# Kernel optimization log

Hardware: AMD Instinct MI355X
Metric: run time of the kernel (lower is better)

## Reference

```python
import jax, jax.numpy as jnp
import numpy as np

N = 100000      # nodes
E = 1600000     # edges
D_IN = 128
D_H = 128
D_OUT = 32
NUM_LAYERS = 3


def setup_inputs() -> dict:
    key = jax.random.key(0)
    ks = jax.random.split(key, 12)
    x = jax.random.normal(ks[0], (N, D_IN), dtype=jnp.float32)
    edge_index = jax.random.randint(ks[1], (2, E), 0, N, dtype=jnp.int64)
    def lin(k, fan_in, fan_out):
        bound = 1.0 / np.sqrt(fan_in)
        kw, kb = jax.random.split(k)
        W = jax.random.uniform(kw, (fan_in, fan_out), jnp.float32, -bound, bound)
        b = jax.random.uniform(kb, (fan_out,), jnp.float32, -bound, bound)
        return W, b
    W0, b0 = lin(ks[2], D_IN, D_H)
    W1, b1 = lin(ks[3], D_H, D_H)
    W2, b2 = lin(ks[4], D_H, D_H)
    Wfc, bfc = lin(ks[5], D_H, D_OUT)
    return {"x": x, "edge_index": edge_index, "W0": W0, "b0": b0,
            "W1": W1, "b1": b1, "W2": W2, "b2": b2, "Wfc": Wfc, "bfc": bfc}


def reference(x, edge_index, W0, b0, W1, b1, W2, b2, Wfc, bfc):
    n = x.shape[0]
    # add self-loops once (PyG GCNConv default add_self_loops=True)
    loop = jnp.arange(n, dtype=edge_index.dtype)
    src = jnp.concatenate([edge_index[0], loop])  # [E+N]
    dst = jnp.concatenate([edge_index[1], loop])
    # symmetric degree normalization: deg computed over destination (col)
    deg = jax.ops.segment_sum(jnp.ones_like(dst, dtype=x.dtype), dst, num_segments=n)
    dis = jnp.where(deg > 0, jax.lax.rsqrt(deg), 0.0)  # deg^{-1/2}, inf->0
    norm = (dis[src] * dis[dst])[:, None]              # [E+N, 1]

    def gcn_conv(h, W, b):
        h = h @ W                                       # [N, d_out]
        agg = jax.ops.segment_sum(h[src] * norm, dst, num_segments=n)
        return agg + b                                  # bias after aggregation

    h = x
    for (W, b) in ((W0, b0), (W1, b1), (W2, b2)):
        h = jax.nn.relu(gcn_conv(h, W, b))              # dropout p=0 -> identity
    pooled = jnp.mean(h, axis=0)                        # [D_H]
    return pooled @ Wfc + bfc                           # [D_OUT]
```

## Files before the change

### kernel.cpp

```cpp
#include <hip/hip_runtime.h>
#include <hip/hip_bf16.h>
#include <cstdint>


typedef unsigned short u16;
typedef unsigned int u32;
typedef unsigned char u8;
typedef __attribute__((ext_vector_type(8))) short short8v;
typedef __attribute__((ext_vector_type(4))) float f32x4;
typedef __attribute__((ext_vector_type(2))) float f32x2;

#define NBMAX 256
#define BKSH  9
#define SCH   2048
#define CAP   12288

__device__ inline u16 f2bf(float f) {
  u32 u = __float_as_uint(f);
  u += 0x7fff + ((u >> 16) & 1);
  return (u16)(u >> 16);
}
__device__ inline float bflo(u32 u) { return __uint_as_float(u << 16); }
__device__ inline float bfhi(u32 u) { return __uint_as_float(u & 0xffff0000u); }

__global__ void k_init(const int* __restrict__ ei, int* __restrict__ mode,
                       int* __restrict__ bucketCur, float* __restrict__ pooled,
                       int e, int nb) {
  if (blockIdx.x == 0) {
    __shared__ int any;
    if (threadIdx.x == 0) any = 0;
    __syncthreads();
    int lim = min(e, 2048);
    int local = 0;
    for (int i = threadIdx.x; i < lim; i += blockDim.x)
      local |= (ei[2 * i + 1] != 0);
    if (local) atomicOr(&any, 1);
    __syncthreads();
    if (threadIdx.x == 0) mode[0] = (any == 0) ? 1 : 0;
  } else {
    int i = threadIdx.x;
    if (i < nb) bucketCur[i] = 0;
    if (i < 128) pooled[i] = 0.0f;
  }
}

__global__ __launch_bounds__(256) void b_scatter(const int* __restrict__ ei,
                                                 const int* __restrict__ mode,
                                                 int* __restrict__ bucketCur,
                                                 int* __restrict__ pairBuf,
                                                 int e, int nb) {
  __shared__ int cnt[NBMAX];
  __shared__ int pre[NBMAX];
  __shared__ int base[NBMAX];
  __shared__ int stage[2 * SCH];
  const int t = threadIdx.x;
  const int chunk0 = blockIdx.x * SCH;
  const int nloc = min(SCH, e - chunk0);
  const int m = mode[0];

  cnt[t] = 0;
  __syncthreads();

  int myS[SCH / 256], myD[SCH / 256], myB[SCH / 256], mySlot[SCH / 256];
#pragma unroll
  for (int j = 0; j < SCH / 256; ++j) {
    int li = j * 256 + t;
    myB[j] = -1;
    if (li < nloc) {
      int i = chunk0 + li;
      long long di = (long long)e + i;
      int s = m ? ei[2 * (long long)i] : ei[i];
      int d = m ? ei[2 * di] : ei[di];
      int b = d >> BKSH;
      myS[j] = s; myD[j] = d; myB[j] = b;
      mySlot[j] = atomicAdd(&cnt[b], 1);
    }
  }
  __syncthreads();

  int c0 = cnt[t];
  pre[t] = c0;
  __syncthreads();
  for (int d = 1; d < NBMAX; d <<= 1) {
    int v = (t >= d) ? pre[t - d] : 0;
    __syncthreads();
    pre[t] += v;
    __syncthreads();
  }
  int myPre = pre[t] - c0;
  if (t < nb && c0 > 0) base[t] = atomicAdd(&bucketCur[t], c0);
  __syncthreads();
  cnt[t] = myPre;
  __syncthreads();

#pragma unroll
  for (int j = 0; j < SCH / 256; ++j) {
    if (myB[j] >= 0) {
      int si = cnt[myB[j]] + mySlot[j];
      stage[2 * si] = myS[j];
      stage[2 * si + 1] = myD[j];
    }
  }
  __syncthreads();

  int wave = t >> 6, lane = t & 63;
  for (int b = wave; b < nb; b += 4) {
    int cb = pre[b] - cnt[b];
    if (cb <= 0) continue;
    int lo = cnt[b];
    int gb = base[b];
    int room = CAP - gb;
    int allowed = (room > 0) ? min(cb, room) : 0;
    size_t dst = ((size_t)b * CAP + gb) * 2;
    for (int j = lane; j < 2 * allowed; j += 64)
      pairBuf[dst + j] = stage[2 * lo + j];
  }
}

__global__ __launch_bounds__(256) void b_bscan2(const int* __restrict__ bucketCur,
                                                int* __restrict__ bucketOff, int nb) {
  __shared__ int sh[NBMAX];
  int t = threadIdx.x;
  int c = (t < nb) ? bucketCur[t] : 0;
  sh[t] = c;
  __syncthreads();
  for (int d = 1; d < NBMAX; d <<= 1) {
    int v = (t >= d) ? sh[t - d] : 0;
    __syncthreads();
    sh[t] += v;
    __syncthreads();
  }
  if (t < nb) bucketOff[t] = sh[t] - c;
}

__global__ __launch_bounds__(512) void b_fine(const int* __restrict__ pairBuf,
                                              const int* __restrict__ bucketCur,
                                              const int* __restrict__ bucketOff,
                                              int* __restrict__ offs,
                                              float* __restrict__ dis,
                                              int* __restrict__ csr,
                                              int n, int e) {
  const int b = blockIdx.x;
  const int d0 = b << BKSH;
  const size_t pb = (size_t)b * CAP;
  const int cnt = bucketCur[b];
  const int lo = bucketOff[b];
  __shared__ int arr[1 << BKSH];
  __shared__ int cur[1 << BKSH];
  const int t = threadIdx.x;
  arr[t] = 0; cur[t] = 0;
  __syncthreads();
  for (int i = t; i < cnt; i += 512) {
    int d = pairBuf[2 * (pb + i) + 1];
    atomicAdd(&arr[d - d0], 1);
  }
  __syncthreads();
  int c0 = arr[t];
  __syncthreads();
  for (int dd = 1; dd < 512; dd <<= 1) {
    int v = (t >= dd) ? arr[t - dd] : 0;
    __syncthreads();
    arr[t] += v;
    __syncthreads();
  }
  int epre = arr[t] - c0;
  int gd = d0 + t;
  if (gd < n) {
    offs[gd] = lo + epre;
    dis[gd] = rsqrtf((float)c0 + 1.0f);
  }
  __syncthreads();
  arr[t] = epre;
  __syncthreads();
  for (int i = t; i < cnt; i += 512) {
    int s = pairBuf[2 * (pb + i)];
    int d = pairBuf[2 * (pb + i) + 1];
    int ld = d - d0;
    int p = lo + arr[ld] + atomicAdd(&cur[ld], 1);
    csr[p] = s;
  }
  if (b == 0 && t == 0) offs[n] = e;
}

__global__ __launch_bounds__(256) void k_wpack3(const float* __restrict__ W0,
                                                const float* __restrict__ W1,
                                                const float* __restrict__ W2,
                                                u16* __restrict__ wp) {
  int f = blockIdx.x * 256 + threadIdx.x;
  int wsel = f >> 11;
  int li = f & 2047;
  const float* W = (wsel == 0) ? W0 : (wsel == 1) ? W1 : W2;
  u16* dst = wp + (size_t)wsel * 2048 * 8;
  int ct = li >> 8, kc = (li >> 6) & 3, lane = li & 63;
  int g = lane >> 4, c = lane & 15;
  u32 o[4];
#pragma unroll
  for (int q = 0; q < 4; ++q) {
    int k = kc * 32 + g * 8 + q * 2;
    u16 e0 = f2bf(W[(size_t)k * 128 + ct * 16 + c]);
    u16 e1 = f2bf(W[(size_t)(k + 1) * 128 + ct * 16 + c]);
    o[q] = (u32)e0 | ((u32)e1 << 16);
  }
  uint4 v; v.x = o[0]; v.y = o[1]; v.z = o[2]; v.w = o[3];
  *reinterpret_cast<uint4*>(dst + (size_t)li * 8) = v;
}

template <bool FP32IN>
__global__ __launch_bounds__(256) void k_gemm_mfma(const void* __restrict__ hin,
                                                   const u16* __restrict__ wp,
                                                   const float* __restrict__ dis,
                                                   u8* __restrict__ tmpf8, int n) {
  __shared__ float eps[64 * 132];
  const int tid = threadIdx.x;
  const int w = tid >> 6, l = tid & 63;
  const int g = l >> 4, c16 = l & 15;
  const int rowbase = blockIdx.x * 64 + w * 16;

  const short8v zero8 = {0, 0, 0, 0, 0, 0, 0, 0};
  short8v a[4];
  int ar = rowbase + c16;
  bool aok = ar < n;
#pragma unroll
  for (int kc = 0; kc < 4; ++kc) {
    if (FP32IN) {
      const float* hrow = (const float*)hin + (size_t)ar * 128;
      short8v s = zero8;
      if (aok) {
        float4 v0 = *reinterpret_cast<const float4*>(hrow + kc * 32 + g * 8);
        float4 v1 = *reinterpret_cast<const float4*>(hrow + kc * 32 + g * 8 + 4);
        s[0] = (short)f2bf(v0.x); s[1] = (short)f2bf(v0.y);
        s[2] = (short)f2bf(v0.z); s[3] = (short)f2bf(v0.w);
        s[4] = (short)f2bf(v1.x); s[5] = (short)f2bf(v1.y);
        s[6] = (short)f2bf(v1.z); s[7] = (short)f2bf(v1.w);
      }
      a[kc] = s;
    } else {
      const u16* hrow = (const u16*)hin + (size_t)ar * 128;
      a[kc] = aok ? *reinterpret_cast<const short8v*>(hrow + kc * 32 + g * 8) : zero8;
    }
  }

  f32x4 acc[8];
#pragma unroll
  for (int ct = 0; ct < 8; ++ct) acc[ct] = f32x4{0.f, 0.f, 0.f, 0.f};

#pragma unroll
  for (int ct = 0; ct < 8; ++ct) {
#pragma unroll
    for (int kc = 0; kc < 4; ++kc) {
      short8v b = *reinterpret_cast<const short8v*>(wp + ((size_t)(ct * 4 + kc) * 64 + l) * 8);
      acc[ct] = __builtin_amdgcn_mfma_f32_16x16x32_bf16(a[kc], b, acc[ct], 0, 0, 0);
    }
  }

#pragma unroll
  for (int j = 0; j < 4; ++j) {
    int rl = w * 16 + g * 4 + j;
    int gr = blockIdx.x * 64 + rl;
    float dn = (gr < n) ? dis[gr] * 16.0f : 0.f;
#pragma unroll
    for (int ct = 0; ct < 8; ++ct)
      eps[rl * 132 + ct * 16 + c16] = acc[ct][j] * dn;
  }
  __syncthreads();

  int rl = tid >> 2, seg = tid & 3;
  int gr = blockIdx.x * 64 + rl;
  if (gr < n) {
    const float* src = &eps[rl * 132 + seg * 32];
    u32 wds[8];
#pragma unroll
    for (int q = 0; q < 4; ++q) {
      float4 v0 = *reinterpret_cast<const float4*>(src + q * 8);
      float4 v1 = *reinterpret_cast<const float4*>(src + q * 8 + 4);
      int p0 = __builtin_amdgcn_cvt_pk_fp8_f32(v0.x, v0.y, 0, false);
      p0 = __builtin_amdgcn_cvt_pk_fp8_f32(v0.z, v0.w, p0, true);
      int p1 = __builtin_amdgcn_cvt_pk_fp8_f32(v1.x, v1.y, 0, false);
      p1 = __builtin_amdgcn_cvt_pk_fp8_f32(v1.z, v1.w, p1, true);
      wds[q * 2] = (u32)p0;
      wds[q * 2 + 1] = (u32)p1;
    }
    uint4 o0; o0.x = wds[0]; o0.y = wds[1]; o0.z = wds[2]; o0.w = wds[3];
    uint4 o1; o1.x = wds[4]; o1.y = wds[5]; o1.z = wds[6]; o1.w = wds[7];
    *reinterpret_cast<uint4*>(tmpf8 + (size_t)gr * 128 + seg * 32) = o0;
    *reinterpret_cast<uint4*>(tmpf8 + (size_t)gr * 128 + seg * 32 + 16) = o1;
  }
}

__global__ __launch_bounds__(256) void k_gather_f8(const u8* __restrict__ tmpf8,
                                                   const int* __restrict__ csr,
                                                   const int* __restrict__ offs,
                                                   const float* __restrict__ dis,
                                                   const float* __restrict__ bias,
                                                   u16* __restrict__ houtb, int n) {
  int node0 = (blockIdx.x * 4 + (threadIdx.x >> 6)) * 4;
  if (node0 >= n) return;
  int lane = threadIdx.x & 63;
  int q = lane >> 4, l16 = lane & 15;
  const uint2* tp = reinterpret_cast<const uint2*>(tmpf8) + l16;

  int s_[5];
#pragma unroll
  for (int k = 0; k < 5; ++k)
    s_[k] = __builtin_amdgcn_readfirstlane(offs[min(node0 + k, n)]);
  int len01 = max(s_[1] - s_[0], s_[2] - s_[1]);
  int len23 = max(s_[3] - s_[2], s_[4] - s_[3]);
  int nbatch = (max(len01, len23) + 7) >> 3;
  int gmax = max(s_[4] - 1, 0);

  int myStart = (q == 0) ? s_[0] : (q == 1) ? s_[1] : (q == 2) ? s_[2] : s_[3];
  int myEnd   = (q == 0) ? s_[1] : (q == 1) ? s_[2] : (q == 2) ? s_[3] : s_[4];
  int myNode = min(node0 + q, n - 1);
  bool doWrite = (node0 + q) < n;

  f32x4 aL[2], aH[2];
#pragma unroll
  for (int i = 0; i < 2; ++i) { aL[i] = f32x4{0,0,0,0}; aH[i] = f32x4{0,0,0,0}; }

  {
    uint2 v = tp[(u32)myNode << 4];
    f32x2 l0 = __builtin_amdgcn_cvt_pk_f32_fp8((int)v.x, false);
    f32x2 h0 = __builtin_amdgcn_cvt_pk_f32_fp8((int)v.x, true);
    f32x2 l1 = __builtin_amdgcn_cvt_pk_f32_fp8((int)v.y, false);
    f32x2 h1 = __builtin_amdgcn_cvt_pk_f32_fp8((int)v.y, true);
    aL[0] += f32x4{l0.x, l0.y, h0.x, h0.y};
    aH[0] += f32x4{l1.x, l1.y, h1.x, h1.y};
  }

  for (int b = 0; b < nbatch; ++b) {
    int eb = b * 8;
    u32 ro[8];
    float sel[8];
#pragma unroll
    for (int j = 0; j < 8; ++j) {
      int r0 = __builtin_amdgcn_readfirstlane(csr[min(s_[0] + eb + j, gmax)]);
      int r1 = __builtin_amdgcn_readfirstlane(csr[min(s_[1] + eb + j, gmax)]);
      int r2 = __builtin_amdgcn_readfirstlane(csr[min(s_[2] + eb + j, gmax)]);
      int r3 = __builtin_amdgcn_readfirstlane(csr[min(s_[3] + eb + j, gmax)]);
      int rr = (q == 0) ? r0 : (q == 1) ? r1 : (q == 2) ? r2 : r3;
      ro[j] = (u32)rr << 4;
      sel[j] = (myStart + eb + j < myEnd) ? 1.0f : 0.0f;
    }
    uint2 v[8];
#pragma unroll
    for (int j = 0; j < 8; ++j) v[j] = tp[ro[j]];
#pragma unroll
    for (int j = 0; j < 8; ++j) {
      f32x2 l0 = __builtin_amdgcn_cvt_pk_f32_fp8((int)v[j].x, false);
      f32x2 h0 = __builtin_amdgcn_cvt_pk_f32_fp8((int)v[j].x, true);
      f32x2 l1 = __builtin_amdgcn_cvt_pk_f32_fp8((int)v[j].y, false);
      f32x2 h1 = __builtin_amdgcn_cvt_pk_f32_fp8((int)v[j].y, true);
      aL[j & 1] += f32x4{l0.x, l0.y, h0.x, h0.y} * sel[j];
      aH[j & 1] += f32x4{l1.x, l1.y, h1.x, h1.y} * sel[j];
    }
  }

  f32x4 sL = aL[0] + aL[1];
  f32x4 sH = aH[0] + aH[1];
  float dn = dis[myNode] * 0.0625f;
  float4 b0v = reinterpret_cast<const float4*>(bias)[l16 * 2];
  float4 b1v = reinterpret_cast<const float4*>(bias)[l16 * 2 + 1];
  float r0 = fmaf(dn, sL.x, b0v.x); r0 = r0 > 0.f ? r0 : 0.f;
  float r1 = fmaf(dn, sL.y, b0v.y); r1 = r1 > 0.f ? r1 : 0.f;
  float r2 = fmaf(dn, sL.z, b0v.z); r2 = r2 > 0.f ? r2 : 0.f;
  float r3 = fmaf(dn, sL.w, b0v.w); r3 = r3 > 0.f ? r3 : 0.f;
  float r4 = fmaf(dn, sH.x, b1v.x); r4 = r4 > 0.f ? r4 : 0.f;
  float r5 = fmaf(dn, sH.y, b1v.y); r5 = r5 > 0.f ? r5 : 0.f;
  float r6 = fmaf(dn, sH.z, b1v.z); r6 = r6 > 0.f ? r6 : 0.f;
  float r7 = fmaf(dn, sH.w, b1v.w); r7 = r7 > 0.f ? r7 : 0.f;
  if (doWrite) {
    uint4 o;
    o.x = (u32)f2bf(r0) | ((u32)f2bf(r1) << 16);
    o.y = (u32)f2bf(r2) | ((u32)f2bf(r3) << 16);
    o.z = (u32)f2bf(r4) | ((u32)f2bf(r5) << 16);
    o.w = (u32)f2bf(r6) | ((u32)f2bf(r7) << 16);
    reinterpret_cast<uint4*>(houtb)[(size_t)myNode * 16 + l16] = o;
  }
}

__global__ __launch_bounds__(256) void k_pool_bf(const u16* __restrict__ h,
                                                 float* __restrict__ pooled, int n) {
  int lane = threadIdx.x & 63, wv = threadIdx.x >> 6;
  const u32* hp = reinterpret_cast<const u32*>(h);
  float sx = 0.f, sy = 0.f;
  for (int r = blockIdx.x * 4 + wv; r < n; r += gridDim.x * 4) {
    u32 u = hp[(size_t)r * 64 + lane];
    sx += bflo(u); sy += bfhi(u);
  }
  __shared__ float red[2][256];
  red[0][threadIdx.x] = sx;
  red[1][threadIdx.x] = sy;
  __syncthreads();
  if (threadIdx.x < 64) {
    float tx = red[0][threadIdx.x] + red[0][threadIdx.x + 64] +
               red[0][threadIdx.x + 128] + red[0][threadIdx.x + 192];
    float ty = red[1][threadIdx.x] + red[1][threadIdx.x + 64] +
               red[1][threadIdx.x + 128] + red[1][threadIdx.x + 192];
    atomicAdd(&pooled[threadIdx.x * 2], tx);
    atomicAdd(&pooled[threadIdx.x * 2 + 1], ty);
  }
}

__global__ void k_final(const float* __restrict__ pooled, const float* __restrict__ Wfc,
                        const float* __restrict__ bfc, float* __restrict__ out,
                        float invn) {
  int j = threadIdx.x;
  if (j < 32) {
    float acc = 0.f;
    for (int k = 0; k < 128; ++k) acc = fmaf(pooled[k], Wfc[k * 32 + j], acc);
    out[j] = fmaf(acc, invn, bfc[j]);
  }
}

extern "C" void kernel_launch(void* const* d_in, const int* in_sizes, int n_in,
                              void* d_out, int out_size, void* d_ws, size_t ws_size,
                              hipStream_t stream) {
  const float* x   = (const float*)d_in[0];
  const int*   ei  = (const int*)d_in[1];
  const float* W0  = (const float*)d_in[2];
  const float* b0  = (const float*)d_in[3];
  const float* W1  = (const float*)d_in[4];
  const float* b1  = (const float*)d_in[5];
  const float* W2  = (const float*)d_in[6];
  const float* b2  = (const float*)d_in[7];
  const float* Wfc = (const float*)d_in[8];
  const float* bfc = (const float*)d_in[9];

  const int n = in_sizes[0] / 128;
  const int e = in_sizes[1] / 2;
  const int nb = (n + (1 << BKSH) - 1) >> BKSH;

  char* ws = (char*)d_ws;
  size_t off = 0;
  auto alloc = [&](size_t bytes) -> void* {
    void* p = ws + off;
    off = (off + bytes + 255) & ~(size_t)255;
    return p;
  };
  int*   mode      = (int*)alloc(sizeof(int));
  int*   bucketCur = (int*)alloc(NBMAX * 4);
  int*   bucketOff = (int*)alloc((NBMAX + 1) * 4);
  int*   offs      = (int*)alloc((size_t)(n + 1) * 4);
  float* dis       = (float*)alloc((size_t)n * 4);
  int*   csr       = (int*)alloc((size_t)e * 4);
  float* pooled    = (float*)alloc(128 * 4);
  u16*   wp        = (u16*)alloc(3 * 2048 * 8 * 2);
  u8*    tmpf8     = (u8*)alloc((size_t)n * 128);
  u16*   houtb     = (u16*)alloc((size_t)n * 128 * 2);
  int*   pairBuf   = (int*)houtb;

  k_init<<<2, 256, 0, stream>>>(ei, mode, bucketCur, pooled, e, nb);
  b_scatter<<<(e + SCH - 1) / SCH, 256, 0, stream>>>(ei, mode, bucketCur, pairBuf, e, nb);
  b_bscan2<<<1, 256, 0, stream>>>(bucketCur, bucketOff, nb);
  b_fine<<<nb, 512, 0, stream>>>(pairBuf, bucketCur, bucketOff, offs, dis, csr, n, e);

  k_wpack3<<<24, 256, 0, stream>>>(W0, W1, W2, wp);

  int gg = (n + 63) / 64;
  int gn = (n + 15) / 16;

  k_gemm_mfma<true><<<gg, 256, 0, stream>>>(x, wp, dis, tmpf8, n);
  k_gather_f8<<<gn, 256, 0, stream>>>(tmpf8, csr, offs, dis, b0, houtb, n);
  k_gemm_mfma<false><<<gg, 256, 0, stream>>>(houtb, wp + 2048 * 8, dis, tmpf8, n);
  k_gather_f8<<<gn, 256, 0, stream>>>(tmpf8, csr, offs, dis, b1, houtb, n);
  k_gemm_mfma<false><<<gg, 256, 0, stream>>>(houtb, wp + 2 * 2048 * 8, dis, tmpf8, n);
  k_gather_f8<<<gn, 256, 0, stream>>>(tmpf8, csr, offs, dis, b2, houtb, n);

  k_pool_bf<<<512, 256, 0, stream>>>(houtb, pooled, n);
  k_final<<<1, 32, 0, stream>>>(pooled, Wfc, bfc, (float*)d_out, 1.0f / (float)n);
}
```

Measured before the change: 295.7 us.

## Fuse pooling into final gather, pack edge pairs, merge scan and weight-pack kernels

Weight packing moves into the init kernel and the bucket-offset scan is recomputed inside each b_fine block, removing two launches. Edge pairs are packed into one u32 (18-bit source, 9-bit local destination), halving scatter and fine-sort traffic but limiting node count to 2^18. The final gather layer accumulates per-block column sums in shared memory and skips writing bf16 activations; a small reduce kernel replaces the separate pooling pass. This adds shared-memory atomics in the last gather and an extra partials buffer.

```diff
diff --git a/kernel.cpp b/kernel.cpp
--- a/kernel.cpp
+++ b/kernel.cpp
@@ -23,10 +23,17 @@
 __device__ inline float bflo(u32 u) { return __uint_as_float(u << 16); }
 __device__ inline float bfhi(u32 u) { return __uint_as_float(u & 0xffff0000u); }
 
-__global__ void k_init(const int* __restrict__ ei, int* __restrict__ mode,
-                       int* __restrict__ bucketCur, float* __restrict__ pooled,
-                       int e, int nb) {
-  if (blockIdx.x == 0) {
+__global__ __launch_bounds__(256) void k_init(const int* __restrict__ ei,
+                                              int* __restrict__ mode,
+                                              int* __restrict__ bucketCur,
+                                              float* __restrict__ pooled,
+                                              const float* __restrict__ W0,
+                                              const float* __restrict__ W1,
+                                              const float* __restrict__ W2,
+                                              u16* __restrict__ wp,
+                                              int e, int nb) {
+  int bid = blockIdx.x;
+  if (bid == 0) {
     __shared__ int any;
     if (threadIdx.x == 0) any = 0;
     __syncthreads();
@@ -37,22 +44,40 @@
     if (local) atomicOr(&any, 1);
     __syncthreads();
     if (threadIdx.x == 0) mode[0] = (any == 0) ? 1 : 0;
-  } else {
+  } else if (bid == 1) {
     int i = threadIdx.x;
     if (i < nb) bucketCur[i] = 0;
     if (i < 128) pooled[i] = 0.0f;
+  } else {
+    int f = (bid - 2) * 256 + threadIdx.x;
+    int wsel = f >> 11;
+    int li = f & 2047;
+    const float* W = (wsel == 0) ? W0 : (wsel == 1) ? W1 : W2;
+    u16* dst = wp + (size_t)wsel * 2048 * 8;
+    int ct = li >> 8, kc = (li >> 6) & 3, lane = li & 63;
+    int g = lane >> 4, c = lane & 15;
+    u32 o[4];
+#pragma unroll
+    for (int q = 0; q < 4; ++q) {
+      int k = kc * 32 + g * 8 + q * 2;
+      u16 e0 = f2bf(W[(size_t)k * 128 + ct * 16 + c]);
+      u16 e1 = f2bf(W[(size_t)(k + 1) * 128 + ct * 16 + c]);
+      o[q] = (u32)e0 | ((u32)e1 << 16);
+    }
+    uint4 v; v.x = o[0]; v.y = o[1]; v.z = o[2]; v.w = o[3];
+    *reinterpret_cast<uint4*>(dst + (size_t)li * 8) = v;
   }
 }
 
 __global__ __launch_bounds__(256) void b_scatter(const int* __restrict__ ei,
                                                  const int* __restrict__ mode,
                                                  int* __restrict__ bucketCur,
-                                                 int* __restrict__ pairBuf,
+                                                 u32* __restrict__ pairBuf,
                                                  int e, int nb) {
   __shared__ int cnt[NBMAX];
   __shared__ int pre[NBMAX];
   __shared__ int base[NBMAX];
-  __shared__ int stage[2 * SCH];
+  __shared__ u32 stage[SCH];
   const int t = threadIdx.x;
   const int chunk0 = blockIdx.x * SCH;
   const int nloc = min(SCH, e - chunk0);
@@ -61,7 +86,8 @@
   cnt[t] = 0;
   __syncthreads();
 
-  int myS[SCH / 256], myD[SCH / 256], myB[SCH / 256], mySlot[SCH / 256];
+  u32 myP[SCH / 256];
+  int myB[SCH / 256], mySlot[SCH / 256];
 #pragma unroll
   for (int j = 0; j < SCH / 256; ++j) {
     int li = j * 256 + t;
@@ -72,7 +98,8 @@
       int s = m ? ei[2 * (long long)i] : ei[i];
       int d = m ? ei[2 * di] : ei[di];
       int b = d >> BKSH;
-      myS[j] = s; myD[j] = d; myB[j] = b;
+      myP[j] = (u32)s | ((u32)(d & ((1 << BKSH) - 1)) << 18);
+      myB[j] = b;
       mySlot[j] = atomicAdd(&cnt[b], 1);
     }
   }
@@ -95,11 +122,8 @@
 
 #pragma unroll
   for (int j = 0; j < SCH / 256; ++j) {
-    if (myB[j] >= 0) {
-      int si = cnt[myB[j]] + mySlot[j];
-      stage[2 * si] = myS[j];
-      stage[2 * si + 1] = myD[j];
-    }
+    if (myB[j] >= 0)
+      stage[cnt[myB[j]] + mySlot[j]] = myP[j];
   }
   __syncthreads();
 
@@ -111,48 +135,42 @@
     int gb = base[b];
     int room = CAP - gb;
     int allowed = (room > 0) ? min(cb, room) : 0;
-    size_t dst = ((size_t)b * CAP + gb) * 2;
-    for (int j = lane; j < 2 * allowed; j += 64)
-      pairBuf[dst + j] = stage[2 * lo + j];
-  }
-}
-
-__global__ __launch_bounds__(256) void b_bscan2(const int* __restrict__ bucketCur,
-                                                int* __restrict__ bucketOff, int nb) {
-  __shared__ int sh[NBMAX];
-  int t = threadIdx.x;
-  int c = (t < nb) ? bucketCur[t] : 0;
-  sh[t] = c;
-  __syncthreads();
-  for (int d = 1; d < NBMAX; d <<= 1) {
-    int v = (t >= d) ? sh[t - d] : 0;
-    __syncthreads();
-    sh[t] += v;
-    __syncthreads();
-  }
-  if (t < nb) bucketOff[t] = sh[t] - c;
-}
-
-__global__ __launch_bounds__(512) void b_fine(const int* __restrict__ pairBuf,
+    size_t dst = (size_t)b * CAP + gb;
+    for (int j = lane; j < allowed; j += 64)
+      pairBuf[dst + j] = stage[lo + j];
+  }
+}
+
+__global__ __launch_bounds__(512) void b_fine(const u32* __restrict__ pairBuf,
                                               const int* __restrict__ bucketCur,
-                                              const int* __restrict__ bucketOff,
                                               int* __restrict__ offs,
                                               float* __restrict__ dis,
                                               int* __restrict__ csr,
-                                              int n, int e) {
+                                              int n, int e, int nb) {
   const int b = blockIdx.x;
   const int d0 = b << BKSH;
   const size_t pb = (size_t)b * CAP;
   const int cnt = bucketCur[b];
-  const int lo = bucketOff[b];
+  __shared__ int bc[NBMAX];
   __shared__ int arr[1 << BKSH];
   __shared__ int cur[1 << BKSH];
   const int t = threadIdx.x;
+
+  if (t < NBMAX) bc[t] = (t < nb) ? bucketCur[t] : 0;
+  __syncthreads();
+  for (int d = 1; d < NBMAX; d <<= 1) {
+    int v = (t < NBMAX && t >= d) ? bc[t - d] : 0;
+    __syncthreads();
+    if (t < NBMAX) bc[t] += v;
+    __syncthreads();
+  }
+  const int lo = (b == 0) ? 0 : bc[b - 1];
+
   arr[t] = 0; cur[t] = 0;
   __syncthreads();
   for (int i = t; i < cnt; i += 512) {
-    int d = pairBuf[2 * (pb + i) + 1];
-    atomicAdd(&arr[d - d0], 1);
+    u32 v = pairBuf[pb + i];
+    atomicAdd(&arr[v >> 18], 1);
   }
   __syncthreads();
   int c0 = arr[t];
@@ -173,36 +191,12 @@
   arr[t] = epre;
   __syncthreads();
   for (int i = t; i < cnt; i += 512) {
-    int s = pairBuf[2 * (pb + i)];
-    int d = pairBuf[2 * (pb + i) + 1];
-    int ld = d - d0;
+    u32 v = pairBuf[pb + i];
+    int ld = v >> 18;
     int p = lo + arr[ld] + atomicAdd(&cur[ld], 1);
-    csr[p] = s;
+    csr[p] = (int)(v & 0x3FFFFu);
   }
   if (b == 0 && t == 0) offs[n] = e;
-}
-
-__global__ __launch_bounds__(256) void k_wpack3(const float* __restrict__ W0,
-                                                const float* __restrict__ W1,
-                                                const float* __restrict__ W2,
-                                                u16* __restrict__ wp) {
-  int f = blockIdx.x * 256 + threadIdx.x;
-  int wsel = f >> 11;
-  int li = f & 2047;
-  const float* W = (wsel == 0) ? W0 : (wsel == 1) ? W1 : W2;
-  u16* dst = wp + (size_t)wsel * 2048 * 8;
-  int ct = li >> 8, kc = (li >> 6) & 3, lane = li & 63;
-  int g = lane >> 4, c = lane & 15;
-  u32 o[4];
-#pragma unroll
-  for (int q = 0; q < 4; ++q) {
-    int k = kc * 32 + g * 8 + q * 2;
-    u16 e0 = f2bf(W[(size_t)k * 128 + ct * 16 + c]);
-    u16 e1 = f2bf(W[(size_t)(k + 1) * 128 + ct * 16 + c]);
-    o[q] = (u32)e0 | ((u32)e1 << 16);
-  }
-  uint4 v; v.x = o[0]; v.y = o[1]; v.z = o[2]; v.w = o[3];
-  *reinterpret_cast<uint4*>(dst + (size_t)li * 8) = v;
 }
 
 template <bool FP32IN>
@@ -287,14 +281,22 @@
   }
 }
 
+template <bool POOL>
 __global__ __launch_bounds__(256) void k_gather_f8(const u8* __restrict__ tmpf8,
                                                    const int* __restrict__ csr,
                                                    const int* __restrict__ offs,
                                                    const float* __restrict__ dis,
                                                    const float* __restrict__ bias,
-                                                   u16* __restrict__ houtb, int n) {
+                                                   u16* __restrict__ houtb,
+                                                   float* __restrict__ partials,
+                                                   int n) {
+  __shared__ float pp[128];
   int node0 = (blockIdx.x * 4 + (threadIdx.x >> 6)) * 4;
-  if (node0 >= n) return;
+  if (!POOL && node0 >= n) return;
+  if (POOL) {
+    if (threadIdx.x < 128) pp[threadIdx.x] = 0.f;
+    __syncthreads();
+  }
   int lane = threadIdx.x & 63;
   int q = lane >> 4, l16 = lane & 15;
   const uint2* tp = reinterpret_cast<const uint2*>(tmpf8) + l16;
@@ -368,37 +370,37 @@
   float r5 = fmaf(dn, sH.y, b1v.y); r5 = r5 > 0.f ? r5 : 0.f;
   float r6 = fmaf(dn, sH.z, b1v.z); r6 = r6 > 0.f ? r6 : 0.f;
   float r7 = fmaf(dn, sH.w, b1v.w); r7 = r7 > 0.f ? r7 : 0.f;
-  if (doWrite) {
-    uint4 o;
-    o.x = (u32)f2bf(r0) | ((u32)f2bf(r1) << 16);
-    o.y = (u32)f2bf(r2) | ((u32)f2bf(r3) << 16);
-    o.z = (u32)f2bf(r4) | ((u32)f2bf(r5) << 16);
-    o.w = (u32)f2bf(r6) | ((u32)f2bf(r7) << 16);
-    reinterpret_cast<uint4*>(houtb)[(size_t)myNode * 16 + l16] = o;
-  }
-}
-
-__global__ __launch_bounds__(256) void k_pool_bf(const u16* __restrict__ h,
-                                                 float* __restrict__ pooled, int n) {
-  int lane = threadIdx.x & 63, wv = threadIdx.x >> 6;
-  const u32* hp = reinterpret_cast<const u32*>(h);
-  float sx = 0.f, sy = 0.f;
-  for (int r = blockIdx.x * 4 + wv; r < n; r += gridDim.x * 4) {
-    u32 u = hp[(size_t)r * 64 + lane];
-    sx += bflo(u); sy += bfhi(u);
-  }
-  __shared__ float red[2][256];
-  red[0][threadIdx.x] = sx;
-  red[1][threadIdx.x] = sy;
-  __syncthreads();
-  if (threadIdx.x < 64) {
-    float tx = red[0][threadIdx.x] + red[0][threadIdx.x + 64] +
-               red[0][threadIdx.x + 128] + red[0][threadIdx.x + 192];
-    float ty = red[1][threadIdx.x] + red[1][threadIdx.x + 64] +
-               red[1][threadIdx.x + 128] + red[1][threadIdx.x + 192];
-    atomicAdd(&pooled[threadIdx.x * 2], tx);
-    atomicAdd(&pooled[threadIdx.x * 2 + 1], ty);
-  }
+
+  if (!POOL) {
+    if (doWrite) {
+      uint4 o;
+      o.x = (u32)f2bf(r0) | ((u32)f2bf(r1) << 16);
+      o.y = (u32)f2bf(r2) | ((u32)f2bf(r3) << 16);
+      o.z = (u32)f2bf(r4) | ((u32)f2bf(r5) << 16);
+      o.w = (u32)f2bf(r6) | ((u32)f2bf(r7) << 16);
+      reinterpret_cast<uint4*>(houtb)[(size_t)myNode * 16 + l16] = o;
+    }
+  } else {
+    if (doWrite) {
+      int c = l16 * 8;
+      atomicAdd(&pp[c + 0], r0); atomicAdd(&pp[c + 1], r1);
+      atomicAdd(&pp[c + 2], r2); atomicAdd(&pp[c + 3], r3);
+      atomicAdd(&pp[c + 4], r4); atomicAdd(&pp[c + 5], r5);
+      atomicAdd(&pp[c + 6], r6); atomicAdd(&pp[c + 7], r7);
+    }
+    __syncthreads();
+    if (threadIdx.x < 128)
+      partials[(size_t)blockIdx.x * 128 + threadIdx.x] = pp[threadIdx.x];
+  }
+}
+
+__global__ __launch_bounds__(128) void k_pred(const float* __restrict__ partials,
+                                              float* __restrict__ pooled, int nrow) {
+  int c = threadIdx.x;
+  float acc = 0.f;
+  for (int r = blockIdx.x; r < nrow; r += gridDim.x)
+    acc += partials[(size_t)r * 128 + c];
+  atomicAdd(&pooled[c], acc);
 }
 
 __global__ void k_final(const float* __restrict__ pooled, const float* __restrict__ Wfc,
@@ -439,7 +441,6 @@
   };
   int*   mode      = (int*)alloc(sizeof(int));
   int*   bucketCur = (int*)alloc(NBMAX * 4);
-  int*   bucketOff = (int*)alloc((NBMAX + 1) * 4);
   int*   offs      = (int*)alloc((size_t)(n + 1) * 4);
   float* dis       = (float*)alloc((size_t)n * 4);
   int*   csr       = (int*)alloc((size_t)e * 4);
@@ -447,25 +448,23 @@
   u16*   wp        = (u16*)alloc(3 * 2048 * 8 * 2);
   u8*    tmpf8     = (u8*)alloc((size_t)n * 128);
   u16*   houtb     = (u16*)alloc((size_t)n * 128 * 2);
-  int*   pairBuf   = (int*)houtb;
-
-  k_init<<<2, 256, 0, stream>>>(ei, mode, bucketCur, pooled, e, nb);
+  int    gn        = (n + 15) / 16;
+  float* partials  = (float*)alloc((size_t)gn * 128 * 4);
+  u32*   pairBuf   = (u32*)houtb;
+
+  k_init<<<26, 256, 0, stream>>>(ei, mode, bucketCur, pooled, W0, W1, W2, wp, e, nb);
   b_scatter<<<(e + SCH - 1) / SCH, 256, 0, stream>>>(ei, mode, bucketCur, pairBuf, e, nb);
-  b_bscan2<<<1, 256, 0, stream>>>(bucketCur, bucketOff, nb);
-  b_fine<<<nb, 512, 0, stream>>>(pairBuf, bucketCur, bucketOff, offs, dis, csr, n, e);
-
-  k_wpack3<<<24, 256, 0, stream>>>(W0, W1, W2, wp);
+  b_fine<<<nb, 512, 0, stream>>>(pairBuf, bucketCur, offs, dis, csr, n, e, nb);
 
   int gg = (n + 63) / 64;
-  int gn = (n + 15) / 16;
 
   k_gemm_mfma<true><<<gg, 256, 0, stream>>>(x, wp, dis, tmpf8, n);
-  k_gather_f8<<<gn, 256, 0, stream>>>(tmpf8, csr, offs, dis, b0, houtb, n);
+  k_gather_f8<false><<<gn, 256, 0, stream>>>(tmpf8, csr, offs, dis, b0, houtb, partials, n);
   k_gemm_mfma<false><<<gg, 256, 0, stream>>>(houtb, wp + 2048 * 8, dis, tmpf8, n);
-  k_gather_f8<<<gn, 256, 0, stream>>>(tmpf8, csr, offs, dis, b1, houtb, n);
+  k_gather_f8<false><<<gn, 256, 0, stream>>>(tmpf8, csr, offs, dis, b1, houtb, partials, n);
   k_gemm_mfma<false><<<gg, 256, 0, stream>>>(houtb, wp + 2 * 2048 * 8, dis, tmpf8, n);
-  k_gather_f8<<<gn, 256, 0, stream>>>(tmpf8, csr, offs, dis, b2, houtb, n);
-
-  k_pool_bf<<<512, 256, 0, stream>>>(houtb, pooled, n);
+  k_gather_f8<true><<<gn, 256, 0, stream>>>(tmpf8, csr, offs, dis, b2, houtb, partials, n);
+
+  k_pred<<<64, 128, 0, stream>>>(partials, pooled, gn);
   k_final<<<1, 32, 0, stream>>>(pooled, Wfc, bfc, (float*)d_out, 1.0f / (float)n);
 }
```

New measurement: 321.0 us. 1.09x slower.
